# Kernel tuning notes

Measured on AMD Instinct MI355X. Metric: run time of the kernel, lower is better.

Reference implementation:

```python
import jax, jax.numpy as jnp
from jax import lax
import numpy as np

INPUT_SIZE = 64
HIDDEN = 16
SEQ_LEN = 512
NUM_CLASSES = 6
BATCH = 1024


def setup_inputs() -> dict:
    key = jax.random.key(0)
    ks = jax.random.split(key, 7)
    s_ih = 1.0 / np.sqrt(HIDDEN)
    return {
        "x": jax.random.normal(ks[0], (BATCH, SEQ_LEN, INPUT_SIZE), dtype=jnp.float32),
        # PyTorch LSTM params: gate order [i, f, g, o]
        "w_ih": jax.random.uniform(ks[1], (4 * HIDDEN, INPUT_SIZE), minval=-s_ih, maxval=s_ih, dtype=jnp.float32),
        "w_hh": jax.random.uniform(ks[2], (4 * HIDDEN, HIDDEN), minval=-s_ih, maxval=s_ih, dtype=jnp.float32),
        "b_ih": jax.random.uniform(ks[3], (4 * HIDDEN,), minval=-s_ih, maxval=s_ih, dtype=jnp.float32),
        "b_hh": jax.random.uniform(ks[4], (4 * HIDDEN,), minval=-s_ih, maxval=s_ih, dtype=jnp.float32),
        "w_fc": jax.random.uniform(ks[5], (NUM_CLASSES, HIDDEN * SEQ_LEN),
                                   minval=-1.0 / np.sqrt(HIDDEN * SEQ_LEN),
                                   maxval=1.0 / np.sqrt(HIDDEN * SEQ_LEN), dtype=jnp.float32),
        "b_fc": jax.random.uniform(ks[6], (NUM_CLASSES,),
                                   minval=-1.0 / np.sqrt(HIDDEN * SEQ_LEN),
                                   maxval=1.0 / np.sqrt(HIDDEN * SEQ_LEN), dtype=jnp.float32),
    }


def reference(x, w_ih, w_hh, b_ih, b_hh, w_fc, b_fc):
    B, T, _ = x.shape
    H = w_hh.shape[1]
    # Precompute input contribution to all gates: [B, T, 4H]
    gates_x = jnp.einsum("bti,gi->btg", x, w_ih) + b_ih + b_hh
    gates_t = jnp.swapaxes(gates_x, 0, 1)  # [T, B, 4H] for scan

    def step(carry, gx):
        h, c = carry
        g = gx + h @ w_hh.T  # [B, 4H]
        i, f, gg, o = jnp.split(g, 4, axis=-1)
        c = jax.nn.sigmoid(f) * c + jax.nn.sigmoid(i) * jnp.tanh(gg)
        h = jax.nn.sigmoid(o) * jnp.tanh(c)
        return (h, c), h

    h0 = jnp.zeros((B, H), x.dtype)
    _, hs = lax.scan(step, (h0, h0), gates_t)  # hs: [T, B, H]
    out = jnp.swapaxes(hs, 0, 1).reshape(B, T * H)  # flatten per batch_first reshape
    return out @ w_fc.T + b_fc
```

## Files before the change

### kernel.cpp

```cpp
#include <hip/hip_runtime.h>
#include <stdint.h>

#define SEQ   512
#define NB    1024
#define NIN   64
#define NH    16
#define NCLS  6

typedef __attribute__((ext_vector_type(8))) short short8;
typedef __attribute__((ext_vector_type(4))) float f32x4;

__device__ __forceinline__ float sigfast(float z) {
    return __builtin_amdgcn_rcpf(1.f + __builtin_amdgcn_exp2f(z * -1.4426950408889634f));
}

__device__ __forceinline__ float readlane_f(float v, int l) {
    return __int_as_float(__builtin_amdgcn_readlane(__float_as_int(v), l));
}

__device__ __forceinline__ void split8(float4 u0, float4 u1, short8& hi, short8& lo) {
    float f[8] = {u0.x, u0.y, u0.z, u0.w, u1.x, u1.y, u1.z, u1.w};
    #pragma unroll
    for (int j = 0; j < 8; ++j) {
        uint32_t b = __float_as_uint(f[j]);
        uint16_t hb = (uint16_t)(b >> 16);
        hi[j] = (short)hb;
        float hf = __uint_as_float(((uint32_t)hb) << 16);
        lo[j] = (short)(uint16_t)(__float_as_uint(f[j] - hf) >> 16);
    }
}

#define GSTRIDE 20

__global__ __launch_bounds__(256, 1)
void lstm_fused_kernel(const float* __restrict__ x,
                       const float* __restrict__ w_ih,
                       const float* __restrict__ w_hh,
                       const float* __restrict__ b_ih,
                       const float* __restrict__ b_hh,
                       const float* __restrict__ w_fc,
                       const float* __restrict__ b_fc,
                       float* __restrict__ out)
{
    __shared__ float stageG[4][64 * GSTRIDE];
    __shared__ float stageHT[4][256];

    const int tid  = threadIdx.x;
    const int wid  = tid >> 6;
    const int lane = tid & 63;
    const int b    = blockIdx.x * 4 + wid;

    const int ml   = lane & 15;
    const int half = lane >> 4;
    const int kk   = half * 8;

    short8 Bh[4][2], Bl[4][2];
    #pragma unroll
    for (int tau = 0; tau < 4; ++tau) {
        #pragma unroll
        for (int ch = 0; ch < 2; ++ch) {
            const float* wr = w_ih + (tau * 16 + ml) * NIN + ch * 32 + kk;
            float4 u0 = *(const float4*)wr;
            float4 u1 = *(const float4*)(wr + 4);
            split8(u0, u1, Bh[tau][ch], Bl[tau][ch]);
        }
    }

    float whh[NH];
    #pragma unroll
    for (int j = 0; j < NH; j += 4) {
        float4 u = *(const float4*)(w_hh + lane * NH + j);
        whh[j] = u.x; whh[j+1] = u.y; whh[j+2] = u.z; whh[j+3] = u.w;
    }
    const float bias = b_ih[lane] + b_hh[lane];

    const bool isg  = (lane >= 32) && (lane < 48);
    const float sA  = isg ? 2.f : 1.f;
    const float sB  = isg ? -1.f : 0.f;

    float c_state = 0.f;
    float hs[NH];
    #pragma unroll
    for (int j = 0; j < NH; ++j) hs[j] = 0.f;
    float accfc[NCLS];
    #pragma unroll
    for (int cls = 0; cls < NCLS; ++cls) accfc[cls] = 0.f;

    const float* xbase = x + ((size_t)b * SEQ + ml) * NIN + kk;
    float4 px0 = *(const float4*)(xbase + 0);
    float4 px1 = *(const float4*)(xbase + 4);
    float4 px2 = *(const float4*)(xbase + 32);
    float4 px3 = *(const float4*)(xbase + 36);

    const int u = lane & 15;

    for (int grp = 0; grp < SEQ / 16; ++grp) {
        float4 wf[NCLS];
        #pragma unroll
        for (int cls = 0; cls < NCLS; ++cls)
            wf[cls] = *(const float4*)(w_fc + cls * (SEQ * NH) + grp * 256 + lane * 4);

        short8 a0h, a0l, a1h, a1l;
        split8(px0, px1, a0h, a0l);
        split8(px2, px3, a1h, a1l);

        if (grp < SEQ / 16 - 1) {
            const float* xp = xbase + (size_t)(grp + 1) * 16 * NIN;
            px0 = *(const float4*)(xp + 0);
            px1 = *(const float4*)(xp + 4);
            px2 = *(const float4*)(xp + 32);
            px3 = *(const float4*)(xp + 36);
        }

        f32x4 acc[4];
        #pragma unroll
        for (int tau = 0; tau < 4; ++tau) {
            f32x4 c_ = {0.f, 0.f, 0.f, 0.f};
            c_ = __builtin_amdgcn_mfma_f32_16x16x32_bf16(a0h, Bh[tau][0], c_, 0, 0, 0);
            c_ = __builtin_amdgcn_mfma_f32_16x16x32_bf16(a1h, Bh[tau][1], c_, 0, 0, 0);
            c_ = __builtin_amdgcn_mfma_f32_16x16x32_bf16(a0l, Bh[tau][0], c_, 0, 0, 0);
            c_ = __builtin_amdgcn_mfma_f32_16x16x32_bf16(a0h, Bl[tau][0], c_, 0, 0, 0);
            c_ = __builtin_amdgcn_mfma_f32_16x16x32_bf16(a1l, Bh[tau][1], c_, 0, 0, 0);
            c_ = __builtin_amdgcn_mfma_f32_16x16x32_bf16(a1h, Bl[tau][1], c_, 0, 0, 0);
            acc[tau] = c_;
        }

        #pragma unroll
        for (int tau = 0; tau < 4; ++tau) {
            *(f32x4*)&stageG[wid][(tau * 16 + ml) * GSTRIDE + half * 4] = acc[tau];
        }
        __builtin_amdgcn_s_waitcnt(0xC07F);

        float gvv[16];
        #pragma unroll
        for (int q = 0; q < 4; ++q) {
            f32x4 g4 = *(f32x4*)&stageG[wid][lane * GSTRIDE + q * 4];
            gvv[q*4+0] = g4[0]; gvv[q*4+1] = g4[1]; gvv[q*4+2] = g4[2]; gvv[q*4+3] = g4[3];
        }

        #pragma unroll
        for (int r = 0; r < 16; ++r) {
            float q0 = fmaf(hs[0], whh[0], gvv[r] + bias);
            float q1 = hs[1] * whh[1];
            float q2 = hs[2] * whh[2];
            float q3 = hs[3] * whh[3];
            #pragma unroll
            for (int j = 4; j < NH; j += 4) {
                q0 = fmaf(hs[j+0], whh[j+0], q0);
                q1 = fmaf(hs[j+1], whh[j+1], q1);
                q2 = fmaf(hs[j+2], whh[j+2], q2);
                q3 = fmaf(hs[j+3], whh[j+3], q3);
            }
            const float gate = (q0 + q1) + (q2 + q3);

            const float act = fmaf(sA, sigfast(sA * gate), sB);

            const float ig = __shfl(act, u);
            const float fg = __shfl(act, u + 16);
            const float gg = __shfl(act, u + 32);
            const float og = __shfl(act, u + 48);

            c_state = fmaf(fg, c_state, ig * gg);
            const float th = fmaf(2.f, sigfast(2.f * c_state), -1.f);
            const float hn = og * th;

            if (lane < NH) stageHT[wid][r * NH + lane] = hn;

            #pragma unroll
            for (int j = 0; j < NH; ++j) hs[j] = readlane_f(hn, j);
        }
        __builtin_amdgcn_s_waitcnt(0xC07F);

        {
            float4 h4 = *(float4*)&stageHT[wid][lane * 4];
            #pragma unroll
            for (int cls = 0; cls < NCLS; ++cls) {
                accfc[cls] = fmaf(h4.x, wf[cls].x, accfc[cls]);
                accfc[cls] = fmaf(h4.y, wf[cls].y, accfc[cls]);
                accfc[cls] = fmaf(h4.z, wf[cls].z, accfc[cls]);
                accfc[cls] = fmaf(h4.w, wf[cls].w, accfc[cls]);
            }
        }
    }

    #pragma unroll
    for (int cls = 0; cls < NCLS; ++cls) {
        float v = accfc[cls];
        v += __shfl_xor(v, 1);
        v += __shfl_xor(v, 2);
        v += __shfl_xor(v, 4);
        v += __shfl_xor(v, 8);
        v += __shfl_xor(v, 16);
        v += __shfl_xor(v, 32);
        accfc[cls] = v;
    }
    if (lane == 0) {
        #pragma unroll
        for (int cls = 0; cls < NCLS; ++cls)
            out[b * NCLS + cls] = accfc[cls] + b_fc[cls];
    }
}

extern "C" void kernel_launch(void* const* d_in, const int* in_sizes, int n_in,
                              void* d_out, int out_size, void* d_ws, size_t ws_size,
                              hipStream_t stream) {
    const float* x    = (const float*)d_in[0];
    const float* w_ih = (const float*)d_in[1];
    const float* w_hh = (const float*)d_in[2];
    const float* b_ih = (const float*)d_in[3];
    const float* b_hh = (const float*)d_in[4];
    const float* w_fc = (const float*)d_in[5];
    const float* b_fc = (const float*)d_in[6];
    float* out = (float*)d_out;

    hipLaunchKernelGGL(lstm_fused_kernel, dim3(NB / 4), dim3(256), 0, stream,
                       x, w_ih, w_hh, b_ih, b_hh, w_fc, b_fc, out);
}
```

Measured before the change: 255.5 us.

## Interleave gate rows per hidden unit and use DPP quad broadcasts

Remaps gate rows so that the four gates of each hidden unit sit in adjacent lanes (lane = 4*u + gate). The per-step gate exchange can then use DPP quad_perm broadcasts instead of four ds_bpermute-based __shfl calls on the serial recurrence path. The bias is folded into the MFMA outputs before the LDS store, and the sigmoid scale is precomputed. The hidden-state readlanes and stores are adjusted to the new lane layout.

```diff
diff --git a/kernel.cpp b/kernel.cpp
--- a/kernel.cpp
+++ b/kernel.cpp
@@ -6,13 +6,10 @@
 #define NIN   64
 #define NH    16
 #define NCLS  6
+#define GSTRIDE 20
 
 typedef __attribute__((ext_vector_type(8))) short short8;
 typedef __attribute__((ext_vector_type(4))) float f32x4;
-
-__device__ __forceinline__ float sigfast(float z) {
-    return __builtin_amdgcn_rcpf(1.f + __builtin_amdgcn_exp2f(z * -1.4426950408889634f));
-}
 
 __device__ __forceinline__ float readlane_f(float v, int l) {
     return __int_as_float(__builtin_amdgcn_readlane(__float_as_int(v), l));
@@ -30,7 +27,18 @@
     }
 }
 
-#define GSTRIDE 20
+__device__ __forceinline__ float quad_bcast0(float v) {
+    return __int_as_float(__builtin_amdgcn_update_dpp(0, __float_as_int(v), 0x00, 0xF, 0xF, true));
+}
+__device__ __forceinline__ float quad_bcast1(float v) {
+    return __int_as_float(__builtin_amdgcn_update_dpp(0, __float_as_int(v), 0x55, 0xF, 0xF, true));
+}
+__device__ __forceinline__ float quad_bcast2(float v) {
+    return __int_as_float(__builtin_amdgcn_update_dpp(0, __float_as_int(v), 0xAA, 0xF, 0xF, true));
+}
+__device__ __forceinline__ float quad_bcast3(float v) {
+    return __int_as_float(__builtin_amdgcn_update_dpp(0, __float_as_int(v), 0xFF, 0xF, 0xF, true));
+}
 
 __global__ __launch_bounds__(256, 1)
 void lstm_fused_kernel(const float* __restrict__ x,
@@ -66,17 +74,25 @@
         }
     }
 
+    float bw[4];
+    #pragma unroll
+    for (int tau = 0; tau < 4; ++tau)
+        bw[tau] = b_ih[tau * 16 + ml] + b_hh[tau * 16 + ml];
+
+    const int gate_t = lane & 3;
+    const int u      = lane >> 2;
+    const int grow   = gate_t * 16 + u;
     float whh[NH];
     #pragma unroll
     for (int j = 0; j < NH; j += 4) {
-        float4 u = *(const float4*)(w_hh + lane * NH + j);
-        whh[j] = u.x; whh[j+1] = u.y; whh[j+2] = u.z; whh[j+3] = u.w;
-    }
-    const float bias = b_ih[lane] + b_hh[lane];
-
-    const bool isg  = (lane >= 32) && (lane < 48);
+        float4 w4 = *(const float4*)(w_hh + grow * NH + j);
+        whh[j] = w4.x; whh[j+1] = w4.y; whh[j+2] = w4.z; whh[j+3] = w4.w;
+    }
+
+    const bool  isg = (gate_t == 2);
     const float sA  = isg ? 2.f : 1.f;
     const float sB  = isg ? -1.f : 0.f;
+    const float nk  = sA * -1.4426950408889634f;
 
     float c_state = 0.f;
     float hs[NH];
@@ -91,8 +107,6 @@
     float4 px1 = *(const float4*)(xbase + 4);
     float4 px2 = *(const float4*)(xbase + 32);
     float4 px3 = *(const float4*)(xbase + 36);
-
-    const int u = lane & 15;
 
     for (int grp = 0; grp < SEQ / 16; ++grp) {
         float4 wf[NCLS];
@@ -127,7 +141,9 @@
 
         #pragma unroll
         for (int tau = 0; tau < 4; ++tau) {
-            *(f32x4*)&stageG[wid][(tau * 16 + ml) * GSTRIDE + half * 4] = acc[tau];
+            f32x4 a4 = acc[tau];
+            a4[0] += bw[tau]; a4[1] += bw[tau]; a4[2] += bw[tau]; a4[3] += bw[tau];
+            *(f32x4*)&stageG[wid][(ml * 4 + tau) * GSTRIDE + half * 4] = a4;
         }
         __builtin_amdgcn_s_waitcnt(0xC07F);
 
@@ -140,7 +156,7 @@
 
         #pragma unroll
         for (int r = 0; r < 16; ++r) {
-            float q0 = fmaf(hs[0], whh[0], gvv[r] + bias);
+            float q0 = fmaf(hs[0], whh[0], gvv[r]);
             float q1 = hs[1] * whh[1];
             float q2 = hs[2] * whh[2];
             float q3 = hs[3] * whh[3];
@@ -151,23 +167,25 @@
                 q2 = fmaf(hs[j+2], whh[j+2], q2);
                 q3 = fmaf(hs[j+3], whh[j+3], q3);
             }
-            const float gate = (q0 + q1) + (q2 + q3);
-
-            const float act = fmaf(sA, sigfast(sA * gate), sB);
-
-            const float ig = __shfl(act, u);
-            const float fg = __shfl(act, u + 16);
-            const float gg = __shfl(act, u + 32);
-            const float og = __shfl(act, u + 48);
+            const float gatev = (q0 + q1) + (q2 + q3);
+
+            const float e   = __builtin_amdgcn_exp2f(gatev * nk);
+            const float act = fmaf(sA, __builtin_amdgcn_rcpf(1.f + e), sB);
+
+            const float ig = quad_bcast0(act);
+            const float fg = quad_bcast1(act);
+            const float gg = quad_bcast2(act);
+            const float og = quad_bcast3(act);
 
             c_state = fmaf(fg, c_state, ig * gg);
-            const float th = fmaf(2.f, sigfast(2.f * c_state), -1.f);
+            const float e2 = __builtin_amdgcn_exp2f(c_state * -2.8853900817779268f);
+            const float th = fmaf(2.f, __builtin_amdgcn_rcpf(1.f + e2), -1.f);
             const float hn = og * th;
 
-            if (lane < NH) stageHT[wid][r * NH + lane] = hn;
+            if ((lane & 3) == 0) stageHT[wid][r * NH + u] = hn;
 
             #pragma unroll
-            for (int j = 0; j < NH; ++j) hs[j] = readlane_f(hn, j);
+            for (int j = 0; j < NH; ++j) hs[j] = readlane_f(hn, 4 * j);
         }
         __builtin_amdgcn_s_waitcnt(0xC07F);
 
```

Result: faster. 239.2 us (-6.4%).
